# Optimization experiments

Measured on AMD Instinct MI355X. Metric: run time of the kernel, lower is better.

Reference implementation:

```python
import jax, jax.numpy as jnp
import numpy as np

EPS_IN = 1e-5   # InstanceNorm2d default eps
EPS_VAR = 1e-6  # clamp on attention variance

def instance_norm(x):
    # x: (b, c, h, w); affine=False, biased variance over spatial dims
    mean = jnp.mean(x, axis=(2, 3), keepdims=True)
    var = jnp.var(x, axis=(2, 3), keepdims=True)
    return (x - mean) * jax.lax.rsqrt(var + EPS_IN)

def setup_inputs() -> dict:
    key = jax.random.key(0)
    k1, k2, k3, k4 = jax.random.split(key, 4)
    shp = (4, 512, 64, 64)
    return {
        "c_x": jax.random.normal(k1, shp, dtype=jnp.float32),
        "s_x": jax.random.normal(k2, shp, dtype=jnp.float32),
        "c_1x": jax.random.normal(k3, shp, dtype=jnp.float32),
        "s_1x": jax.random.normal(k4, shp, dtype=jnp.float32),
    }

def reference(c_x, s_x, c_1x, s_1x):
    b, v_dim, h, w = c_x.shape
    hw = h * w
    # Q: (b, hw, qk), K: (b, qk, hw), V: (b, hw, v)
    Q = instance_norm(c_1x).reshape(b, -1, hw).transpose(0, 2, 1)
    K = instance_norm(s_1x).reshape(b, -1, s_1x.shape[2] * s_1x.shape[3])
    V = s_x.reshape(b, v_dim, -1).transpose(0, 2, 1)
    # attention over spatial tokens
    A = jax.nn.softmax(jnp.einsum('bqc,bck->bqk', Q, K), axis=-1)
    M = jnp.einsum('bqk,bkv->bqv', A, V)              # weighted mean
    Var = jnp.einsum('bqk,bkv->bqv', A, V * V) - M * M  # weighted variance
    S = jnp.sqrt(jnp.clip(Var, EPS_VAR, None))
    # back to (b, v, h, w)
    M = M.reshape(b, h, w, -1).transpose(0, 3, 1, 2)
    S = S.reshape(b, h, w, -1).transpose(0, 3, 1, 2)
    return S * instance_norm(c_x) + M
```

## Files before the change

### kernel.cpp

```cpp
#include <hip/hip_runtime.h>
#include <cmath>


#define B_  4
#define C_  512
#define HW_ 4096

typedef _Float16 f16;
typedef _Float16 f16x8 __attribute__((ext_vector_type(8)));
typedef float    f32x4 __attribute__((ext_vector_type(4)));

__device__ __forceinline__ f32x4 mfma16(f16x8 a, f16x8 b, f32x4 c) {
  return __builtin_amdgcn_mfma_f32_16x16x32_f16(a, b, c, 0, 0, 0);
}
__device__ __forceinline__ void g2l16(const f16* g, f16* l) {
  __builtin_amdgcn_global_load_lds(
      (const __attribute__((address_space(1))) void*)g,
      (__attribute__((address_space(3))) void*)l, 16, 0, 0);
}

__global__ __launch_bounds__(256) void k_stats(
    const float* __restrict__ cx, const float* __restrict__ c1,
    const float* __restrict__ s1,
    float2* __restrict__ cxs, float2* __restrict__ c1s, float2* __restrict__ s1s) {
  int c = blockIdx.x, b = blockIdx.y, t = blockIdx.z;
  const float* src = (t == 0 ? cx : (t == 1 ? c1 : s1)) + (size_t)(b * C_ + c) * HW_;
  float s = 0.f, q = 0.f;
  const float4* src4 = (const float4*)src;
  for (int i = threadIdx.x; i < HW_ / 4; i += 256) {
    float4 v = src4[i];
    s += v.x + v.y + v.z + v.w;
    q += v.x * v.x + v.y * v.y + v.z * v.z + v.w * v.w;
  }
#pragma unroll
  for (int off = 1; off < 64; off <<= 1) {
    s += __shfl_xor(s, off);
    q += __shfl_xor(q, off);
  }
  __shared__ float ss[4], sq[4];
  int wv = threadIdx.x >> 6;
  if ((threadIdx.x & 63) == 0) { ss[wv] = s; sq[wv] = q; }
  __syncthreads();
  if (threadIdx.x == 0) {
    float S = ss[0] + ss[1] + ss[2] + ss[3];
    float Q = sq[0] + sq[1] + sq[2] + sq[3];
    float mean = S * (1.f / HW_);
    float var = Q * (1.f / HW_) - mean * mean;
    float2 r;
    r.x = mean;
    r.y = rsqrtf(var + 1e-5f);
    (t == 0 ? cxs : (t == 1 ? c1s : s1s))[b * C_ + c] = r;
  }
}

__global__ __launch_bounds__(256) void k_prept(
    const float* __restrict__ src, const float2* __restrict__ st,
    f16* __restrict__ dst) {
  int pb = blockIdx.x * 64, cb = blockIdx.y * 64, b = blockIdx.z;
  __shared__ float t[64][65];
  int tj = threadIdx.x & 63, tr = threadIdx.x >> 6;
#pragma unroll 4
  for (int p = 0; p < 16; ++p) {
    int cl = p * 4 + tr;
    float2 mr = st[b * C_ + cb + cl];
    float v = src[(size_t)(b * C_ + cb + cl) * HW_ + pb + tj];
    t[cl][tj] = (v - mr.x) * mr.y;
  }
  __syncthreads();
#pragma unroll 4
  for (int p = 0; p < 16; ++p) {
    int pr = p * 4 + tr;
    dst[(size_t)(b * HW_ + pb + pr) * C_ + cb + tj] = (f16)t[tj][pr];
  }
}

__global__ __launch_bounds__(256) void k_prepv(const float* __restrict__ src,
                                               f16* __restrict__ dst) {
  int gid = blockIdx.x * 256 + threadIdx.x;
  const float4* s = (const float4*)src + (size_t)gid * 2;
  float4 v0 = s[0], v1 = s[1];
  f16x8 v = {(f16)v0.x, (f16)v0.y, (f16)v0.z, (f16)v0.w,
             (f16)v1.x, (f16)v1.y, (f16)v1.z, (f16)v1.w};
  *(f16x8*)(dst + (size_t)gid * 8) = v;
}

__global__ __launch_bounds__(256, 2) void k_qk(
    const f16* __restrict__ Qt, const f16* __restrict__ Kt,
    f16* __restrict__ E, float2* __restrict__ mlpart,
    int qspan, int qt128, int npair) {
  int id = blockIdx.x, pair, kt;
  if ((npair & 7) == 0) {
    int xcd = id & 7, j = id >> 3, qrs = npair >> 3;
    pair = xcd * qrs + (j % qrs);
    kt = j / qrs;
  } else {
    pair = id >> 4;
    kt = id & 15;
  }
  int bz = pair / qt128, qt = pair - bz * qt128;

  const f16* Aq = Qt + ((size_t)(bz * qspan + qt * 128)) * C_;
  const f16* Bk = Kt + (size_t)bz * HW_ * C_ + (size_t)kt * 256 * C_;
  f16* Eb = E + ((size_t)(bz * qspan + qt * 128)) * HW_ + kt * 256;
  float2* mlb = mlpart + ((size_t)(bz * qspan + qt * 128)) * 16 + kt;

  __shared__ __align__(16) union ShQK {
    struct { f16 As[128 * 32]; f16 Bs[256 * 32]; } s;
    f16 ebuf[32 * 272];
  } sh;
  __shared__ float sred[2][128];
  f16* As = sh.s.As;
  f16* Bs = sh.s.Bs;

  int t = threadIdx.x, wave = t >> 6, lane = t & 63, lq = lane & 15, quad = lane >> 4;
  int wy = wave >> 1, wx = wave & 1;
  int srow = t >> 2, scol = (t & 3) * 8;

  f32x4 acc[4][8];
#pragma unroll
  for (int mt = 0; mt < 4; ++mt)
#pragma unroll
    for (int nt = 0; nt < 8; ++nt) acc[mt][nt] = (f32x4){0, 0, 0, 0};

  for (int kc = 0; kc < 16; ++kc) {
    __syncthreads();
    g2l16(Aq + (size_t)srow * C_ + kc * 32 + scol, As + t * 8);
    g2l16(Aq + (size_t)(srow + 64) * C_ + kc * 32 + scol, As + 2048 + t * 8);
#pragma unroll
    for (int i = 0; i < 4; ++i)
      g2l16(Bk + (size_t)(srow + 64 * i) * C_ + kc * 32 + scol,
            Bs + i * 2048 + t * 8);
    __syncthreads();
    f16x8 af[4], bf[8];
#pragma unroll
    for (int mt = 0; mt < 4; ++mt)
      af[mt] = *(const f16x8*)(As + (wy * 64 + mt * 16 + lq) * 32 + quad * 8);
#pragma unroll
    for (int nt = 0; nt < 8; ++nt)
      bf[nt] = *(const f16x8*)(Bs + (wx * 128 + nt * 16 + lq) * 32 + quad * 8);
#pragma unroll
    for (int mt = 0; mt < 4; ++mt)
#pragma unroll
      for (int nt = 0; nt < 8; ++nt)
        acc[mt][nt] = mfma16(af[mt], bf[nt], acc[mt][nt]);
  }

#pragma unroll
  for (int mt = 0; mt < 4; ++mt)
#pragma unroll
    for (int r = 0; r < 4; ++r) {
      float v = -1e30f;
#pragma unroll
      for (int nt = 0; nt < 8; ++nt) v = fmaxf(v, acc[mt][nt][r]);
#pragma unroll
      for (int msk = 1; msk < 16; msk <<= 1) v = fmaxf(v, __shfl_xor(v, msk));
      if (lq == 0) sred[wx][wy * 64 + mt * 16 + quad * 4 + r] = v;
    }
  __syncthreads();
  float mrow[4][4];
#pragma unroll
  for (int mt = 0; mt < 4; ++mt)
#pragma unroll
    for (int r = 0; r < 4; ++r) {
      int rr = wy * 64 + mt * 16 + quad * 4 + r;
      mrow[mt][r] = fmaxf(sred[0][rr], sred[1][rr]);
    }

  float rsum[4][4];
#pragma unroll
  for (int mt = 0; mt < 4; ++mt)
#pragma unroll
    for (int r = 0; r < 4; ++r) rsum[mt][r] = 0.f;

#pragma unroll
  for (int mt = 0; mt < 4; ++mt) {
    __syncthreads();
#pragma unroll
    for (int nt = 0; nt < 8; ++nt) {
      f32x4 v = acc[mt][nt];
#pragma unroll
      for (int r = 0; r < 4; ++r) {
        float e = __expf(v[r] - mrow[mt][r]);
        rsum[mt][r] += e;
        sh.ebuf[(wy * 16 + quad * 4 + r) * 272 + wx * 128 + nt * 16 + lq] = (f16)e;
      }
    }
    __syncthreads();
#pragma unroll
    for (int i = 0; i < 4; ++i) {
      int idx = i * 256 + t;
      int rl = idx >> 5, cs = (idx & 31) * 8;
      f16x8 v8 = *(const f16x8*)(sh.ebuf + rl * 272 + cs);
      int grow = (rl >> 4) * 64 + mt * 16 + (rl & 15);
      *(f16x8*)(Eb + (size_t)grow * HW_ + cs) = v8;
    }
  }

#pragma unroll
  for (int mt = 0; mt < 4; ++mt)
#pragma unroll
    for (int r = 0; r < 4; ++r) {
      float v = rsum[mt][r];
#pragma unroll
      for (int msk = 1; msk < 16; msk <<= 1) v += __shfl_xor(v, msk);
      if (lq == 0) sred[wx][wy * 64 + mt * 16 + quad * 4 + r] = v;
    }
  __syncthreads();
  if (wx == 0 && lq == 0) {
#pragma unroll
    for (int mt = 0; mt < 4; ++mt)
#pragma unroll
      for (int r = 0; r < 4; ++r) {
        int rr = wy * 64 + mt * 16 + quad * 4 + r;
        mlb[(size_t)rr * 16] = make_float2(mrow[mt][r], sred[0][rr] + sred[1][rr]);
      }
  }
}

__global__ __launch_bounds__(256) void k_red(const float2* __restrict__ mlpart,
                                             float* __restrict__ alpha) {
  int row = blockIdx.x * 256 + threadIdx.x;
  const float2* p = mlpart + (size_t)row * 16;
  float2 loc[16];
  float m = -1e30f;
#pragma unroll
  for (int i = 0; i < 16; ++i) {
    loc[i] = p[i];
    m = fmaxf(m, loc[i].x);
  }
  float l = 0.f;
#pragma unroll
  for (int i = 0; i < 16; ++i) l += loc[i].y * __expf(loc[i].x - m);
  float invl = 1.f / l;
#pragma unroll
  for (int i = 0; i < 16; ++i)
    alpha[(size_t)row * 16 + i] = __expf(loc[i].x - m) * invl;
}

#define PV_STAGE_A(i)                                                         \
  g2l16(Ap + (size_t)((i)*64 + srow) * HW_ + s2 * 64 + scol,                  \
        sm + pnOff + (i)*4096 + t * 8)
#define PV_STAGE_B(i)                                                         \
  g2l16(Bv + (size_t)((i)*64 + srow) * HW_ + s2 * 64 + scol,                  \
        sm + pnOff + 16384 + (i)*4096 + t * 8)

#define PV_PHASE(MH, NH, STAGE_STMT, POST_STMT)                               \
  {                                                                           \
    f16x8 af00 = *(const f16x8*)(As_s + aoff + ((MH)*2+0)*1024 + cx0);        \
    f16x8 af01 = *(const f16x8*)(As_s + aoff + ((MH)*2+0)*1024 + cx1);        \
    f16x8 af10 = *(const f16x8*)(As_s + aoff + ((MH)*2+1)*1024 + cx0);        \
    f16x8 af11 = *(const f16x8*)(As_s + aoff + ((MH)*2+1)*1024 + cx1);        \
    f16x8 bf00 = *(const f16x8*)(Bs_s + boff + ((NH)*2+0)*1024 + cx0);        \
    f16x8 bf01 = *(const f16x8*)(Bs_s + boff + ((NH)*2+0)*1024 + cx1);        \
    f16x8 bf10 = *(const f16x8*)(Bs_s + boff + ((NH)*2+1)*1024 + cx0);        \
    f16x8 bf11 = *(const f16x8*)(Bs_s + boff + ((NH)*2+1)*1024 + cx1);        \
    STAGE_STMT;                                                               \
    __builtin_amdgcn_s_barrier();                                             \
    asm volatile("s_waitcnt lgkmcnt(0)" ::: "memory");                        \
    __builtin_amdgcn_sched_barrier(0);                                        \
    __builtin_amdgcn_s_setprio(1);                                            \
    af00 *= aal[(MH)*2+0]; af01 *= aal[(MH)*2+0];                             \
    af10 *= aal[(MH)*2+1]; af11 *= aal[(MH)*2+1];                             \
    {                                                                         \
      f16x8 b2;                                                               \
      b2 = bf00 * bf00;                                                       \
      accM [(MH)*2+0][(NH)*2+0] = mfma16(af00, bf00, accM [(MH)*2+0][(NH)*2+0]); \
      accM2[(MH)*2+0][(NH)*2+0] = mfma16(af00, b2,   accM2[(MH)*2+0][(NH)*2+0]); \
      accM [(MH)*2+1][(NH)*2+0] = mfma16(af10, bf00, accM [(MH)*2+1][(NH)*2+0]); \
      accM2[(MH)*2+1][(NH)*2+0] = mfma16(af10, b2,   accM2[(MH)*2+1][(NH)*2+0]); \
      b2 = bf10 * bf10;                                                       \
      accM [(MH)*2+0][(NH)*2+1] = mfma16(af00, bf10, accM [(MH)*2+0][(NH)*2+1]); \
      accM2[(MH)*2+0][(NH)*2+1] = mfma16(af00, b2,   accM2[(MH)*2+0][(NH)*2+1]); \
      accM [(MH)*2+1][(NH)*2+1] = mfma16(af10, bf10, accM [(MH)*2+1][(NH)*2+1]); \
      accM2[(MH)*2+1][(NH)*2+1] = mfma16(af10, b2,   accM2[(MH)*2+1][(NH)*2+1]); \
      b2 = bf01 * bf01;                                                       \
      accM [(MH)*2+0][(NH)*2+0] = mfma16(af01, bf01, accM [(MH)*2+0][(NH)*2+0]); \
      accM2[(MH)*2+0][(NH)*2+0] = mfma16(af01, b2,   accM2[(MH)*2+0][(NH)*2+0]); \
      accM [(MH)*2+1][(NH)*2+0] = mfma16(af11, bf01, accM [(MH)*2+1][(NH)*2+0]); \
      accM2[(MH)*2+1][(NH)*2+0] = mfma16(af11, b2,   accM2[(MH)*2+1][(NH)*2+0]); \
      b2 = bf11 * bf11;                                                       \
      accM [(MH)*2+0][(NH)*2+1] = mfma16(af01, bf11, accM [(MH)*2+0][(NH)*2+1]); \
      accM2[(MH)*2+0][(NH)*2+1] = mfma16(af01, b2,   accM2[(MH)*2+0][(NH)*2+1]); \
      accM [(MH)*2+1][(NH)*2+1] = mfma16(af11, bf11, accM [(MH)*2+1][(NH)*2+1]); \
      accM2[(MH)*2+1][(NH)*2+1] = mfma16(af11, b2,   accM2[(MH)*2+1][(NH)*2+1]); \
    }                                                                         \
    __builtin_amdgcn_s_setprio(0);                                            \
    POST_STMT;                                                                \
    __builtin_amdgcn_s_barrier();                                             \
  }

__global__ __launch_bounds__(512, 2) void k_pv(
    const f16* __restrict__ P, const float* __restrict__ alphaG,
    const f16* __restrict__ V, const float* __restrict__ cx,
    const float2* __restrict__ cxs, float* __restrict__ out,
    int qspan, int qbase, int qt256) {
  int npairs = (int)gridDim.x >> 2;
  int id = blockIdx.x, pair, ct;
  if ((npairs & 7) == 0) {
    int x = id & 7, j = id >> 3, ppx = npairs >> 3;
    pair = x * ppx + (j >> 2);
    ct = j & 3;
  } else {
    pair = id >> 2;
    ct = id & 3;
  }
  int bz = pair / qt256, qt = pair - bz * qt256;

  const f16* Ap = P + ((size_t)(bz * qspan + qt * 256)) * HW_;
  const f16* Bv = V + ((size_t)(bz * C_ + ct * 128)) * HW_;

  __shared__ __align__(16) f16 sm[3 * 24576 + 256 * 17];
  f16* Alh = sm + 3 * 24576;

  int t = threadIdx.x, wave = t >> 6, lane = t & 63, lq = lane & 15, quad = lane >> 4;
  int wy = wave >> 1, wx = wave & 1;

  {
    const float* ag = alphaG + ((size_t)(bz * qspan + qt * 256)) * 16;
#pragma unroll
    for (int i = 0; i < 8; ++i) {
      int e = i * 512 + t;
      Alh[(e >> 4) * 17 + (e & 15)] = (f16)ag[e];
    }
  }

  int srow = t >> 3;
  int scol = ((t & 7) ^ (srow & 7)) * 8;

  int aoff = (wy * 64 + lq) * 64;
  int boff = (wx * 64 + lq) * 64;
  int cx0 = (quad * 8) ^ ((lq & 7) << 3);
  int cx1 = (32 + quad * 8) ^ ((lq & 7) << 3);

  f32x4 accM[4][4], accM2[4][4];
#pragma unroll
  for (int mt = 0; mt < 4; ++mt)
#pragma unroll
    for (int nt = 0; nt < 4; ++nt) {
      accM[mt][nt] = (f32x4){0, 0, 0, 0};
      accM2[mt][nt] = (f32x4){0, 0, 0, 0};
    }

#pragma unroll
  for (int s0 = 0; s0 < 2; ++s0) {
    int off = s0 * 24576;
#pragma unroll
    for (int i = 0; i < 4; ++i)
      g2l16(Ap + (size_t)(i * 64 + srow) * HW_ + s0 * 64 + scol,
            sm + off + i * 4096 + t * 8);
#pragma unroll
    for (int i = 0; i < 2; ++i)
      g2l16(Bv + (size_t)(i * 64 + srow) * HW_ + s0 * 64 + scol,
            sm + off + 16384 + i * 4096 + t * 8);
  }
  asm volatile("s_waitcnt lgkmcnt(0)" ::: "memory");
  asm volatile("s_waitcnt vmcnt(6)" ::: "memory");
  __builtin_amdgcn_s_barrier();

  int ph = 0, pn = 2;
  for (int s = 0; s < 64; ++s) {
    const f16* As_s = sm + ph * 24576;
    const f16* Bs_s = As_s + 16384;
    int pnOff = pn * 24576;
    int s2 = s + 2;
    bool st = s < 62;
    int ktl = s >> 2;
    f16 aal[4];
    aal[0] = Alh[(wy * 64 + lq +  0) * 17 + ktl];
    aal[1] = Alh[(wy * 64 + lq + 16) * 17 + ktl];
    aal[2] = Alh[(wy * 64 + lq + 32) * 17 + ktl];
    aal[3] = Alh[(wy * 64 + lq + 48) * 17 + ktl];

    PV_PHASE(0, 0, if (st) { PV_STAGE_A(0); PV_STAGE_A(1); }, )
    PV_PHASE(0, 1, if (st) { PV_STAGE_A(2); PV_STAGE_A(3); }, )
    PV_PHASE(1, 0, if (st) { PV_STAGE_B(0); }, )
    PV_PHASE(1, 1, if (st) { PV_STAGE_B(1); },
             if (st) { asm volatile("s_waitcnt vmcnt(6)" ::: "memory"); }
             else    { asm volatile("s_waitcnt vmcnt(0)" ::: "memory"); } )

    ph = (ph == 2) ? 0 : ph + 1;
    pn = (pn == 2) ? 0 : pn + 1;
  }

  int chbase = ct * 128 + wx * 64;
#pragma unroll
  for (int mt = 0; mt < 4; ++mt) {
    int q0 = qbase + qt * 256 + wy * 64 + mt * 16 + quad * 4;
#pragma unroll
    for (int nt = 0; nt < 4; ++nt) {
      int c = chbase + nt * 16 + lq;
      float2 stc = cxs[bz * C_ + c];
      size_t base = ((size_t)bz * C_ + c) * HW_ + q0;
      float4 cv = *(const float4*)(cx + base);
      f32x4 m1 = accM[mt][nt], m2 = accM2[mt][nt];
      float4 o;
      o.x = sqrtf(fmaxf(m2[0] - m1[0] * m1[0], 1e-6f)) * ((cv.x - stc.x) * stc.y) + m1[0];
      o.y = sqrtf(fmaxf(m2[1] - m1[1] * m1[1], 1e-6f)) * ((cv.y - stc.x) * stc.y) + m1[1];
      o.z = sqrtf(fmaxf(m2[2] - m1[2] * m1[2], 1e-6f)) * ((cv.z - stc.x) * stc.y) + m1[2];
      o.w = sqrtf(fmaxf(m2[3] - m1[3] * m1[3], 1e-6f)) * ((cv.w - stc.x) * stc.y) + m1[3];
      *(float4*)(out + base) = o;
    }
  }
}

extern "C" void kernel_launch(void* const* d_in, const int* in_sizes, int n_in,
                              void* d_out, int out_size, void* d_ws,
                              size_t ws_size, hipStream_t stream) {
  const float* c_x = (const float*)d_in[0];
  const float* s_x = (const float*)d_in[1];
  const float* c1x = (const float*)d_in[2];
  const float* s1x = (const float*)d_in[3];
  float* out = (float*)d_out;

  char* ws = (char*)d_ws;
  size_t o = 0;
  f16* Qt = (f16*)(ws + o);  o += (size_t)B_ * HW_ * C_ * 2;
  f16* Kt = (f16*)(ws + o);  o += (size_t)B_ * HW_ * C_ * 2;
  f16* Vh = (f16*)(ws + o);  o += (size_t)B_ * HW_ * C_ * 2;
  float2* cxs = (float2*)(ws + o); o += B_ * C_ * sizeof(float2);
  float2* c1s = (float2*)(ws + o); o += B_ * C_ * sizeof(float2);
  float2* s1s = (float2*)(ws + o); o += B_ * C_ * sizeof(float2);
  size_t fixed = (o + 255) & ~(size_t)255;

  const size_t per_row = (size_t)HW_ * 2 + 16 * 8 + 16 * 4;
  struct Cfg { int nb, qs; };
  const Cfg cfgs[5] = {{4, 4096}, {1, 4096}, {1, 2048}, {1, 1024}, {1, 512}};
  Cfg cfg = cfgs[4];
  for (int i = 0; i < 5; ++i) {
    size_t rows = (size_t)cfgs[i].nb * cfgs[i].qs;
    if (fixed + rows * per_row <= ws_size) { cfg = cfgs[i]; break; }
  }
  const int nb = cfg.nb, qspan = cfg.qs, qt128 = qspan / 128, qt256 = qspan / 256;
  const int npair = nb * qt128;
  const int npv = nb * qt256;
  const size_t rows = (size_t)nb * qspan;
  f16* E = (f16*)(ws + fixed);
  float2* mlpart = (float2*)(ws + fixed + rows * HW_ * 2);
  float* alpha = (float*)(ws + fixed + rows * HW_ * 2 + rows * 16 * 8);

  k_stats<<<dim3(C_, B_, 3), 256, 0, stream>>>(c_x, c1x, s1x, cxs, c1s, s1s);
  k_prept<<<dim3(HW_ / 64, C_ / 64, B_), 256, 0, stream>>>(c1x, c1s, Qt);
  k_prept<<<dim3(HW_ / 64, C_ / 64, B_), 256, 0, stream>>>(s1x, s1s, Kt);
  k_prepv<<<dim3(B_ * C_ * HW_ / 8 / 256), 256, 0, stream>>>(s_x, Vh);

  for (int b0 = 0; b0 < B_; b0 += nb) {
    for (int qb = 0; qb < HW_; qb += qspan) {
      const f16* Qtp = Qt + ((size_t)b0 * HW_ + qb) * C_;
      const f16* Ktp = Kt + (size_t)b0 * HW_ * C_;
      const f16* Vp = Vh + (size_t)b0 * C_ * HW_;
      const float* cxp = c_x + (size_t)b0 * C_ * HW_;
      const float2* cxsp = cxs + b0 * C_;
      float* outp = out + (size_t)b0 * C_ * HW_;

      k_qk<<<dim3((unsigned)(npair * 16)), 256, 0, stream>>>(
          Qtp, Ktp, E, mlpart, qspan, qt128, npair);
      k_red<<<dim3((unsigned)(rows / 256)), 256, 0, stream>>>(mlpart, alpha);
      k_pv<<<dim3((unsigned)(npv * 4)), 512, 0, stream>>>(
          E, alpha, Vp, cxp, cxsp, outp, qspan, qb, qt256);
    }
  }
}
```

Measured before the change: 431.8 us.

## Restructure PV inner loop into two k-half phases with one barrier

The PV kernel's per-step work is reorganized from four quadrant phases (each computing a 2x2 block of MFMA tiles over both k halves) into two phases that each cover the full 4x4 tile block for one k half. Each phase loads all four A and B fragments once and squares each B fragment once. The per-phase barriers are removed and a single barrier is placed at the end of each k step, cutting eight barriers per iteration to one. Async staging is regrouped into two batches of three loads, which changes how prefetch traffic interleaves with compute. The risk is higher register pressure from holding eight fragments plus four squared fragments, and possible LDS hazards now that the intra-step barriers are gone.

```diff
diff --git a/kernel.cpp b/kernel.cpp
--- a/kernel.cpp
+++ b/kernel.cpp
@@ -244,49 +244,56 @@
   g2l16(Bv + (size_t)((i)*64 + srow) * HW_ + s2 * 64 + scol,                  \
         sm + pnOff + 16384 + (i)*4096 + t * 8)
 
-#define PV_PHASE(MH, NH, STAGE_STMT, POST_STMT)                               \
+#define PV_PHASE(CX, STAGE_STMT, POST_STMT)                                   \
   {                                                                           \
-    f16x8 af00 = *(const f16x8*)(As_s + aoff + ((MH)*2+0)*1024 + cx0);        \
-    f16x8 af01 = *(const f16x8*)(As_s + aoff + ((MH)*2+0)*1024 + cx1);        \
-    f16x8 af10 = *(const f16x8*)(As_s + aoff + ((MH)*2+1)*1024 + cx0);        \
-    f16x8 af11 = *(const f16x8*)(As_s + aoff + ((MH)*2+1)*1024 + cx1);        \
-    f16x8 bf00 = *(const f16x8*)(Bs_s + boff + ((NH)*2+0)*1024 + cx0);        \
-    f16x8 bf01 = *(const f16x8*)(Bs_s + boff + ((NH)*2+0)*1024 + cx1);        \
-    f16x8 bf10 = *(const f16x8*)(Bs_s + boff + ((NH)*2+1)*1024 + cx0);        \
-    f16x8 bf11 = *(const f16x8*)(Bs_s + boff + ((NH)*2+1)*1024 + cx1);        \
+    f16x8 af0 = *(const f16x8*)(As_s + aoff + 0 * 1024 + (CX));               \
+    f16x8 af1 = *(const f16x8*)(As_s + aoff + 1 * 1024 + (CX));               \
+    f16x8 af2 = *(const f16x8*)(As_s + aoff + 2 * 1024 + (CX));               \
+    f16x8 af3 = *(const f16x8*)(As_s + aoff + 3 * 1024 + (CX));               \
+    f16x8 bf0 = *(const f16x8*)(Bs_s + boff + 0 * 1024 + (CX));               \
+    f16x8 bf1 = *(const f16x8*)(Bs_s + boff + 1 * 1024 + (CX));               \
+    f16x8 bf2 = *(const f16x8*)(Bs_s + boff + 2 * 1024 + (CX));               \
+    f16x8 bf3 = *(const f16x8*)(Bs_s + boff + 3 * 1024 + (CX));               \
     STAGE_STMT;                                                               \
-    __builtin_amdgcn_s_barrier();                                             \
     asm volatile("s_waitcnt lgkmcnt(0)" ::: "memory");                        \
     __builtin_amdgcn_sched_barrier(0);                                        \
     __builtin_amdgcn_s_setprio(1);                                            \
-    af00 *= aal[(MH)*2+0]; af01 *= aal[(MH)*2+0];                             \
-    af10 *= aal[(MH)*2+1]; af11 *= aal[(MH)*2+1];                             \
-    {                                                                         \
-      f16x8 b2;                                                               \
-      b2 = bf00 * bf00;                                                       \
-      accM [(MH)*2+0][(NH)*2+0] = mfma16(af00, bf00, accM [(MH)*2+0][(NH)*2+0]); \
-      accM2[(MH)*2+0][(NH)*2+0] = mfma16(af00, b2,   accM2[(MH)*2+0][(NH)*2+0]); \
-      accM [(MH)*2+1][(NH)*2+0] = mfma16(af10, bf00, accM [(MH)*2+1][(NH)*2+0]); \
-      accM2[(MH)*2+1][(NH)*2+0] = mfma16(af10, b2,   accM2[(MH)*2+1][(NH)*2+0]); \
-      b2 = bf10 * bf10;                                                       \
-      accM [(MH)*2+0][(NH)*2+1] = mfma16(af00, bf10, accM [(MH)*2+0][(NH)*2+1]); \
-      accM2[(MH)*2+0][(NH)*2+1] = mfma16(af00, b2,   accM2[(MH)*2+0][(NH)*2+1]); \
-      accM [(MH)*2+1][(NH)*2+1] = mfma16(af10, bf10, accM [(MH)*2+1][(NH)*2+1]); \
-      accM2[(MH)*2+1][(NH)*2+1] = mfma16(af10, b2,   accM2[(MH)*2+1][(NH)*2+1]); \
-      b2 = bf01 * bf01;                                                       \
-      accM [(MH)*2+0][(NH)*2+0] = mfma16(af01, bf01, accM [(MH)*2+0][(NH)*2+0]); \
-      accM2[(MH)*2+0][(NH)*2+0] = mfma16(af01, b2,   accM2[(MH)*2+0][(NH)*2+0]); \
-      accM [(MH)*2+1][(NH)*2+0] = mfma16(af11, bf01, accM [(MH)*2+1][(NH)*2+0]); \
-      accM2[(MH)*2+1][(NH)*2+0] = mfma16(af11, b2,   accM2[(MH)*2+1][(NH)*2+0]); \
-      b2 = bf11 * bf11;                                                       \
-      accM [(MH)*2+0][(NH)*2+1] = mfma16(af01, bf11, accM [(MH)*2+0][(NH)*2+1]); \
-      accM2[(MH)*2+0][(NH)*2+1] = mfma16(af01, b2,   accM2[(MH)*2+0][(NH)*2+1]); \
-      accM [(MH)*2+1][(NH)*2+1] = mfma16(af11, bf11, accM [(MH)*2+1][(NH)*2+1]); \
-      accM2[(MH)*2+1][(NH)*2+1] = mfma16(af11, b2,   accM2[(MH)*2+1][(NH)*2+1]); \
-    }                                                                         \
+    af0 *= aal[0]; af1 *= aal[1]; af2 *= aal[2]; af3 *= aal[3];               \
+    f16x8 q0 = bf0 * bf0, q1 = bf1 * bf1, q2 = bf2 * bf2, q3 = bf3 * bf3;     \
+    accM [0][0] = mfma16(af0, bf0, accM [0][0]);                              \
+    accM2[0][0] = mfma16(af0, q0,  accM2[0][0]);                              \
+    accM [0][1] = mfma16(af0, bf1, accM [0][1]);                              \
+    accM2[0][1] = mfma16(af0, q1,  accM2[0][1]);                              \
+    accM [0][2] = mfma16(af0, bf2, accM [0][2]);                              \
+    accM2[0][2] = mfma16(af0, q2,  accM2[0][2]);                              \
+    accM [0][3] = mfma16(af0, bf3, accM [0][3]);                              \
+    accM2[0][3] = mfma16(af0, q3,  accM2[0][3]);                              \
+    accM [1][0] = mfma16(af1, bf0, accM [1][0]);                              \
+    accM2[1][0] = mfma16(af1, q0,  accM2[1][0]);                              \
+    accM [1][1] = mfma16(af1, bf1, accM [1][1]);                              \
+    accM2[1][1] = mfma16(af1, q1,  accM2[1][1]);                              \
+    accM [1][2] = mfma16(af1, bf2, accM [1][2]);                              \
+    accM2[1][2] = mfma16(af1, q2,  accM2[1][2]);                              \
+    accM [1][3] = mfma16(af1, bf3, accM [1][3]);                              \
+    accM2[1][3] = mfma16(af1, q3,  accM2[1][3]);                              \
+    accM [2][0] = mfma16(af2, bf0, accM [2][0]);                              \
+    accM2[2][0] = mfma16(af2, q0,  accM2[2][0]);                              \
+    accM [2][1] = mfma16(af2, bf1, accM [2][1]);                              \
+    accM2[2][1] = mfma16(af2, q1,  accM2[2][1]);                              \
+    accM [2][2] = mfma16(af2, bf2, accM [2][2]);                              \
+    accM2[2][2] = mfma16(af2, q2,  accM2[2][2]);                              \
+    accM [2][3] = mfma16(af2, bf3, accM [2][3]);                              \
+    accM2[2][3] = mfma16(af2, q3,  accM2[2][3]);                              \
+    accM [3][0] = mfma16(af3, bf0, accM [3][0]);                              \
+    accM2[3][0] = mfma16(af3, q0,  accM2[3][0]);                              \
+    accM [3][1] = mfma16(af3, bf1, accM [3][1]);                              \
+    accM2[3][1] = mfma16(af3, q1,  accM2[3][1]);                              \
+    accM [3][2] = mfma16(af3, bf2, accM [3][2]);                              \
+    accM2[3][2] = mfma16(af3, q2,  accM2[3][2]);                              \
+    accM [3][3] = mfma16(af3, bf3, accM [3][3]);                              \
+    accM2[3][3] = mfma16(af3, q3,  accM2[3][3]);                              \
     __builtin_amdgcn_s_setprio(0);                                            \
     POST_STMT;                                                                \
-    __builtin_amdgcn_s_barrier();                                             \
   }
 
 __global__ __launch_bounds__(512, 2) void k_pv(
@@ -371,12 +378,13 @@
     aal[2] = Alh[(wy * 64 + lq + 32) * 17 + ktl];
     aal[3] = Alh[(wy * 64 + lq + 48) * 17 + ktl];
 
-    PV_PHASE(0, 0, if (st) { PV_STAGE_A(0); PV_STAGE_A(1); }, )
-    PV_PHASE(0, 1, if (st) { PV_STAGE_A(2); PV_STAGE_A(3); }, )
-    PV_PHASE(1, 0, if (st) { PV_STAGE_B(0); }, )
-    PV_PHASE(1, 1, if (st) { PV_STAGE_B(1); },
+    PV_PHASE(cx0,
+             if (st) { PV_STAGE_A(0); PV_STAGE_A(1); PV_STAGE_A(2); }, )
+    PV_PHASE(cx1,
+             if (st) { PV_STAGE_A(3); PV_STAGE_B(0); PV_STAGE_B(1); },
              if (st) { asm volatile("s_waitcnt vmcnt(6)" ::: "memory"); }
-             else    { asm volatile("s_waitcnt vmcnt(0)" ::: "memory"); } )
+             else    { asm volatile("s_waitcnt vmcnt(0)" ::: "memory"); })
+    __builtin_amdgcn_s_barrier();
 
     ph = (ph == 2) ? 0 : ph + 1;
     pn = (pn == 2) ? 0 : pn + 1;
@@ -436,7 +444,7 @@
   const size_t rows = (size_t)nb * qspan;
   f16* E = (f16*)(ws + fixed);
   float2* mlpart = (float2*)(ws + fixed + rows * HW_ * 2);
-  float* alpha = (float*)(ws + fixed + rows * HW_ * 2 + rows * 16 * 8);
+  float* alpha = (float*)(ws + fixed + rows * HW_ * 2 + rows * 16 * 4 * 2);
 
   k_stats<<<dim3(C_, B_, 3), 256, 0, stream>>>(c_x, c1x, s1x, cxs, c1s, s1s);
   k_prept<<<dim3(HW_ / 64, C_ / 64, B_), 256, 0, stream>>>(c1x, c1s, Qt);
```

New measurement: 387.0 us. 10.4% less time.
